# Performance work log

Hardware: AMD Instinct MI355X
Metric: run time of the kernel (lower is better)

The kernel has to match this reference:

```python
import jax, jax.numpy as jnp
import numpy as np

HIDDEN = 2048
N_HEADS = 16
N_KV_HEADS = 4
HEAD_DIM = 128
GROUPS = N_HEADS // N_KV_HEADS
MAX_SEQ = 2048
EPS = 1e-6
ROTARY_DIM = int(HEAD_DIM * 0.5)  # partial_rotary_factor = 0.5
ROPE_THETA = 10000.0


def _rms_norm(x, w):
    xf = x.astype(jnp.float32)
    normed = xf * jax.lax.rsqrt(jnp.mean(xf * xf, axis=-1, keepdims=True) + EPS)
    return (normed * (1.0 + w.astype(jnp.float32))).astype(x.dtype)


def _apply_rotary(x, cos, sin):
    half = x.shape[-1] // 2
    x1, x2 = x[..., :half], x[..., half:]
    return jnp.concatenate([x1 * cos - x2 * sin, x2 * cos + x1 * sin], axis=-1)


def setup_inputs() -> dict:
    key = jax.random.key(0)
    ks = jax.random.split(key, 6)
    s = 0.02
    return {
        "x": jax.random.normal(ks[0], (1, MAX_SEQ, HIDDEN), jnp.float32),
        "input_pos": jnp.arange(MAX_SEQ, dtype=jnp.int32),
        "wq": jax.random.normal(ks[1], (HIDDEN, N_HEADS * HEAD_DIM * 2), jnp.float32) * s,
        "wk": jax.random.normal(ks[2], (HIDDEN, N_KV_HEADS * HEAD_DIM), jnp.float32) * s,
        "wv": jax.random.normal(ks[3], (HIDDEN, N_KV_HEADS * HEAD_DIM), jnp.float32) * s,
        "wo": jax.random.normal(ks[4], (N_HEADS * HEAD_DIM, HIDDEN), jnp.float32) * s,
        "q_norm_w": jnp.zeros((HEAD_DIM,), jnp.float32),
        "k_norm_w": jnp.zeros((HEAD_DIM,), jnp.float32),
    }


def reference(x, input_pos, wq, wk, wv, wo, q_norm_w, k_norm_w):
    B, T, _ = x.shape
    dtype = x.dtype

    qg = (x @ wq).reshape(B, T, N_HEADS, HEAD_DIM * 2)
    q, gate = qg[..., :HEAD_DIM], qg[..., HEAD_DIM:]
    k = (x @ wk).reshape(B, T, N_KV_HEADS, HEAD_DIM)
    v = (x @ wv).reshape(B, T, N_KV_HEADS, HEAD_DIM)

    q = _rms_norm(q, q_norm_w)
    k = _rms_norm(k, k_norm_w)

    # partial RoPE on the first ROTARY_DIM channels of each head
    inv_freq = 1.0 / ROPE_THETA ** (
        jnp.arange(0, ROTARY_DIM, 2, dtype=jnp.float32) / ROTARY_DIM)
    freqs = jnp.outer(input_pos.astype(jnp.float32), inv_freq)  # [T, rd/2]
    cos = jnp.cos(freqs)[:, None, :]  # [T,1,rd/2] broadcast over heads
    sin = jnp.sin(freqs)[:, None, :]
    q = jnp.concatenate(
        [_apply_rotary(q[..., :ROTARY_DIM], cos, sin), q[..., ROTARY_DIM:]], axis=-1)
    k = jnp.concatenate(
        [_apply_rotary(k[..., :ROTARY_DIM], cos, sin), k[..., ROTARY_DIM:]], axis=-1)

    q = q.astype(dtype).transpose(0, 2, 1, 3)  # [B,H,T,D]
    k = k.astype(dtype).transpose(0, 2, 1, 3)  # [B,Hkv,T,D]
    v = v.transpose(0, 2, 1, 3)

    # KV-cache scatter update (cache starts at zeros)
    kc = jnp.zeros((1, N_KV_HEADS, MAX_SEQ, HEAD_DIM), dtype).at[:, :, input_pos].set(k)
    vc = jnp.zeros((1, N_KV_HEADS, MAX_SEQ, HEAD_DIM), dtype).at[:, :, input_pos].set(v)

    # GQA: group query heads instead of materializing repeated K/V
    qg_ = q.reshape(B, N_KV_HEADS, GROUPS, T, HEAD_DIM)
    scale = 1.0 / jnp.sqrt(jnp.asarray(HEAD_DIM, dtype))
    scores = jnp.einsum("bhgtd,bhsd->bhgts", qg_, kc) * scale  # [B,Hkv,G,T,S]

    mask = jnp.tril(jnp.ones((MAX_SEQ, MAX_SEQ), bool))[input_pos]  # [T,S]
    scores = jnp.where(mask[None, None, None], scores, jnp.finfo(scores.dtype).min)
    probs = jax.nn.softmax(scores, axis=-1)

    y = jnp.einsum("bhgts,bhsd->bhgtd", probs, vc)  # [B,Hkv,G,T,D]
    y = y.reshape(B, N_HEADS, T, HEAD_DIM).transpose(0, 2, 1, 3).reshape(B, T, -1)

    y = y * jax.nn.sigmoid(gate.reshape(B, T, -1))
    return y @ wo
```

## Files before the change

kernel.cpp:

```cpp
#include <hip/hip_runtime.h>
#include <cstdint>
#include <cmath>

using u16 = unsigned short;
typedef __attribute__((ext_vector_type(4))) short s16x4;
typedef __attribute__((ext_vector_type(8))) short s16x8;
typedef __attribute__((ext_vector_type(8))) __bf16 bf16x8;
typedef __attribute__((ext_vector_type(4))) float f32x4;

static __device__ __forceinline__ float b2f(u16 u) {
    unsigned int x = ((unsigned int)u) << 16;
    float f; __builtin_memcpy(&f, &x, 4); return f;
}
static __device__ __forceinline__ u16 f2b(float f) {
    unsigned int x; __builtin_memcpy(&x, &f, 4);
    x += 0x7FFFu + ((x >> 16) & 1u);
    return (u16)(x >> 16);
}
static __device__ __forceinline__ bf16x8 as_bf(s16x8 s) {
    return __builtin_bit_cast(bf16x8, s);
}

static __device__ __forceinline__ void stage16(const u16* g, u16* lds_base, int lane) {
#if __has_builtin(__builtin_amdgcn_global_load_lds)
    __builtin_amdgcn_global_load_lds((const __attribute__((address_space(1))) void*)g,
                                     (__attribute__((address_space(3))) void*)lds_base,
                                     16, 0, 0);
#else
    *(s16x8*)(lds_base + (size_t)lane * 8) = *(const s16x8*)g;
#endif
}

__global__ __launch_bounds__(256) void k_wtransAll(const float* __restrict__ wq,
                                                   const float* __restrict__ wk,
                                                   const float* __restrict__ wv,
                                                   const float* __restrict__ wo,
                                                   const float* __restrict__ x,
                                                   u16* __restrict__ wqkvT,
                                                   u16* __restrict__ woT,
                                                   u16* __restrict__ xb) {
    __shared__ u16 tile[64][72];
    int tx = blockIdx.x;
    int tid = threadIdx.x;
    if (tx >= 112) {
        int bid = (tx - 112) * 32 + blockIdx.y;
        int i = bid * 256 + tid;
        const int n4 = 2048 * 2048 / 4;
        const int stride = 1024 * 256;
        for (; i < n4; i += stride) {
            f32x4 v = ((const f32x4*)x)[i];
            s16x4 b;
            for (int j = 0; j < 4; ++j) b[j] = (short)f2b(v[j]);
            ((s16x4*)xb)[i] = b;
        }
        return;
    }
    const float* src; int N, nb, base; u16* dst;
    if (tx < 64)      { src = wq; N = 4096; nb = tx * 64;        base = tx * 64;               dst = wqkvT; }
    else if (tx < 72) { src = wk; N = 512;  nb = (tx - 64) * 64; base = 4096 + (tx - 64) * 64; dst = wqkvT; }
    else if (tx < 80) { src = wv; N = 512;  nb = (tx - 72) * 64; base = 4608 + (tx - 72) * 64; dst = wqkvT; }
    else              { src = wo; N = 2048; nb = (tx - 80) * 64; base = (tx - 80) * 64;        dst = woT; }
    int kb = blockIdx.y * 64;
    int kr = tid >> 2, c0 = (tid & 3) * 16;
#pragma unroll
    for (int i = 0; i < 4; ++i) {
        f32x4 v = *(const f32x4*)(src + (size_t)(kb + kr) * N + nb + c0 + i * 4);
        s16x4 b;
        for (int j = 0; j < 4; ++j) b[j] = (short)f2b(v[j]);
        *(s16x4*)&tile[kr][c0 + i * 4] = b;
    }
    __syncthreads();
    int nr = tid >> 2, k0 = (tid & 3) * 16;
    s16x8 v0, v1;
    for (int j = 0; j < 8; ++j) { v0[j] = (short)tile[k0 + j][nr]; v1[j] = (short)tile[k0 + 8 + j][nr]; }
    *(s16x8*)(dst + (size_t)(base + nr) * 2048 + kb + k0) = v0;
    *(s16x8*)(dst + (size_t)(base + nr) * 2048 + kb + k0 + 8) = v1;
}

template <bool OUT_F32>
__global__ __launch_bounds__(256) void k_gemm_bt(const u16* __restrict__ A,
                                                 const u16* __restrict__ Bt,
                                                 void* __restrict__ Cv,
                                                 int M, int N, int K) {
    __shared__ u16 As[128 * 64];
    __shared__ u16 Bs[128 * 64];
    int nx = gridDim.x, ny = gridDim.y;
    int flat = blockIdx.y * nx + blockIdx.x;
    int xcd = flat & 7, i = flat >> 3;
    int P = nx >> 3;
    int bnl = i / ny;
    int bmi = i - bnl * ny;
    if (bnl & 1) bmi = ny - 1 - bmi;
    int bn = (xcd * P + bnl) * 128;
    int bm = bmi * 128;

    int tid = threadIdx.x, wid = tid >> 6, lane = tid & 63;
    int l15 = lane & 15, g = lane >> 4;
    int wr = (wid >> 1) * 64, wc = (wid & 1) * 64;
    f32x4 acc[4][4];
    for (int ii = 0; ii < 4; ++ii) for (int j = 0; j < 4; ++j) acc[ii][j] = f32x4{0.f, 0.f, 0.f, 0.f};

    int srow = lane >> 3;
    int scol = ((lane & 7) * 8) ^ (srow << 3);
    const u16* pa = A + (size_t)(bm + srow) * K + scol;
    const u16* pb = Bt + (size_t)(bn + srow) * K + scol;

    for (int kb = 0; kb < K; kb += 64) {
        __syncthreads();
#pragma unroll
        for (int it = 0; it < 4; ++it) {
            int c = it * 4 + wid;
            stage16(pa + (size_t)(c * 8) * K + kb, &As[c * 512], lane);
            stage16(pb + (size_t)(c * 8) * K + kb, &Bs[c * 512], lane);
        }
        __syncthreads();
        int swz = (l15 & 7) << 4;
#pragma unroll
        for (int kk = 0; kk < 64; kk += 32) {
            bf16x8 af[4], bfr[4];
            for (int mi = 0; mi < 4; ++mi) {
                const char* rp = (const char*)As + (wr + mi * 16 + l15) * 128;
                af[mi] = as_bf(*(const s16x8*)(rp + ((kk * 2 + g * 16) ^ swz)));
            }
            for (int ni = 0; ni < 4; ++ni) {
                const char* rp = (const char*)Bs + (wc + ni * 16 + l15) * 128;
                bfr[ni] = as_bf(*(const s16x8*)(rp + ((kk * 2 + g * 16) ^ swz)));
            }
            for (int mi = 0; mi < 4; ++mi)
                for (int ni = 0; ni < 4; ++ni)
                    acc[mi][ni] = __builtin_amdgcn_mfma_f32_16x16x32_bf16(af[mi], bfr[ni], acc[mi][ni], 0, 0, 0);
        }
    }
    for (int mi = 0; mi < 4; ++mi)
        for (int ni = 0; ni < 4; ++ni) {
            int row = bm + wr + mi * 16 + g * 4;
            int col = bn + wc + ni * 16 + l15;
            for (int rr = 0; rr < 4; ++rr) {
                if (OUT_F32)
                    ((float*)Cv)[(size_t)(row + rr) * N + col] = acc[mi][ni][rr];
                else
                    ((u16*)Cv)[(size_t)(row + rr) * N + col] = f2b(acc[mi][ni][rr]);
            }
        }
}

__global__ __launch_bounds__(256) void k_prep_attn(u16* __restrict__ qkv,
                                                   const float* __restrict__ qw,
                                                   const float* __restrict__ kw,
                                                   const int* __restrict__ pos,
                                                   u16* __restrict__ vT) {
    __shared__ u16 tile[64][136];
    int bid = blockIdx.x;
    int tid = threadIdx.x;
    if (bid < 2048) {
        int t = bid, w = tid >> 6, l = tid & 63;
        float fp = (float)pos[t];
        int j = l & 31;
        float invf = __expf(-(float)j * (9.210340371976184f / 32.f));
        float sv, cv;
        sincosf(fp * invf, &sv, &cv);
        for (int task = w; task < 20; task += 4) {
            u16* p; const float* ww;
            if (task < 16) { p = qkv + (size_t)t * 5120 + task * 256; ww = qw; }
            else           { p = qkv + (size_t)t * 5120 + 4096 + (task - 16) * 128; ww = kw; }
            float v0 = b2f(p[l]), v1 = b2f(p[l + 64]);
            float ss = v0 * v0 + v1 * v1;
            for (int m = 32; m; m >>= 1) ss += __shfl_xor(ss, m);
            float rn = rsqrtf(ss * (1.f / 128.f) + 1e-6f);
            float q0 = v0 * rn * (1.f + ww[l]);
            float q1 = v1 * rn * (1.f + ww[l + 64]);
            float other = __shfl_xor(q0, 32);
            float ro = (l < 32) ? (q0 * cv - other * sv) : (q0 * cv + other * sv);
            p[l] = f2b(ro);
            p[l + 64] = f2b(q1);
        }
    } else {
        int r = bid - 2048;
        int tb = (r & 31) * 64, kvh = r >> 5;
        int tr = tid >> 2, c0 = (tid & 3) * 32;
        const u16* src = qkv + (size_t)(tb + tr) * 5120 + 4608 + kvh * 128 + c0;
#pragma unroll
        for (int i = 0; i < 4; ++i)
            *(s16x8*)&tile[tr][c0 + i * 8] = *(const s16x8*)(src + i * 8);
        __syncthreads();
        int d = tid >> 1, t0 = (tid & 1) * 32;
        u16* dst = vT + ((size_t)kvh * 128 + d) * 2048 + tb + t0;
#pragma unroll
        for (int i = 0; i < 4; ++i) {
            s16x8 v;
            for (int j = 0; j < 8; ++j) v[j] = (short)tile[t0 + i * 8 + j][d];
            *(s16x8*)(dst + i * 8) = v;
        }
    }
}

__global__ __launch_bounds__(256) void k_attn_split(const u16* __restrict__ qkv,
                                                    const u16* __restrict__ vT,
                                                    u16* __restrict__ po,
                                                    float* __restrict__ pl) {
    __shared__ u16 Kl[32 * 128];
    __shared__ u16 Vt[128][72];
    __shared__ u16 Pl[4][16][40];
    int head = blockIdx.y, kvh = head >> 2;
    int p = blockIdx.x >> 2, hf = blockIdx.x & 3;
    int tid = threadIdx.x, wid = tid >> 6, lane = tid & 63;
    int l15 = lane & 15, g = lane >> 4;

    for (int sub = 0; sub < 2; ++sub) {
        int qt = sub ? (31 - p) : p;
        int qb0 = qt * 64;
        int nk = (qt + 1) * 2;
        int ktb = (hf * nk) >> 2;
        int kte = ((hf + 1) * nk) >> 2;

        bf16x8 qf[4];
        {
            const u16* qp = qkv + (size_t)(qb0 + wid * 16 + l15) * 5120 + head * 256 + g * 8;
            for (int c = 0; c < 4; ++c) qf[c] = as_bf(*(const s16x8*)(qp + c * 32));
        }
        f32x4 oacc[8];
        for (int nb = 0; nb < 8; ++nb) oacc[nb] = f32x4{0.f, 0.f, 0.f, 0.f};
        float lsum[4] = {0.f, 0.f, 0.f, 0.f};

        for (int kt = ktb; kt < kte; ++kt) {
            int k0 = kt * 32;
            __syncthreads();
            {
#pragma unroll
                for (int i = 0; i < 2; ++i) {
                    int c = (wid << 1) | i;
                    int srow = (c << 2) + (lane >> 4);
                    int bofs = (((lane & 15) << 4) ^ ((srow & 7) << 4));
                    const u16* gs = (const u16*)((const char*)(qkv + (size_t)(k0 + srow) * 5120
                                                               + 4096 + kvh * 128) + bofs);
                    stage16(gs, &Kl[c * 512], lane);
                }
                int vr = tid >> 1, vc0 = (tid & 1) * 16;
                const u16* vs = vT + ((size_t)kvh * 128 + vr) * 2048 + k0 + vc0;
#pragma unroll
                for (int c = 0; c < 2; ++c)
                    *(s16x8*)&Vt[vr][vc0 + 8 * c] = *(const s16x8*)(vs + 8 * c);
            }
            __syncthreads();

            f32x4 sc2[2];
            sc2[0] = f32x4{0.f, 0.f, 0.f, 0.f}; sc2[1] = f32x4{0.f, 0.f, 0.f, 0.f};
            for (int h2 = 0; h2 < 2; ++h2) {
                int krow = h2 * 16 + l15;
                const char* kb_ = (const char*)Kl + krow * 256;
                int sw = (krow & 7) << 4;
                for (int c = 0; c < 4; ++c) {
                    bf16x8 kf = as_bf(*(const s16x8*)(kb_ + ((c * 64 + g * 16) ^ sw)));
                    sc2[h2] = __builtin_amdgcn_mfma_f32_16x16x32_bf16(qf[c], kf, sc2[h2], 0, 0, 0);
                }
            }
            const float scale = 0.08838834764831845f;
            for (int r = 0; r < 4; ++r) {
                int tq = qb0 + wid * 16 + g * 4 + r;
                float pv0 = (k0 + l15 > tq) ? 0.f : __expf(sc2[0][r] * scale);
                float pv1 = (k0 + 16 + l15 > tq) ? 0.f : __expf(sc2[1][r] * scale);
                Pl[wid][g * 4 + r][l15] = f2b(pv0);
                Pl[wid][g * 4 + r][16 + l15] = f2b(pv1);
                lsum[r] += pv0 + pv1;
            }
            bf16x8 pa = as_bf(*(const s16x8*)&Pl[wid][l15][g * 8]);
            for (int nb = 0; nb < 8; ++nb) {
                bf16x8 vb = as_bf(*(const s16x8*)&Vt[nb * 16 + l15][g * 8]);
                oacc[nb] = __builtin_amdgcn_mfma_f32_16x16x32_bf16(pa, vb, oacc[nb], 0, 0, 0);
            }
        }
        u16* pob = po + (size_t)hf * (2048 * 2048);
        float* plb = pl + hf * (16 * 2048) + head * 2048;
        for (int r = 0; r < 4; ++r) {
            float s = lsum[r];
            s += __shfl_xor(s, 1, 16); s += __shfl_xor(s, 2, 16);
            s += __shfl_xor(s, 4, 16); s += __shfl_xor(s, 8, 16);
            int row = qb0 + wid * 16 + g * 4 + r;
            if (l15 == 0) plb[row] = s;
            for (int nb = 0; nb < 8; ++nb)
                pob[(size_t)row * 2048 + head * 128 + nb * 16 + l15] = f2b(oacc[nb][r]);
        }
    }
}

__global__ __launch_bounds__(256) void k_combine(u16* __restrict__ po,
                                                 const float* __restrict__ pl,
                                                 const u16* __restrict__ qkv) {
    int t = blockIdx.x;
    int tid = threadIdx.x;
    int h = tid >> 4, d0 = (tid & 15) * 8;
    const size_t S = (size_t)2048 * 2048;
    const size_t base = (size_t)t * 2048 + h * 128 + d0;
    s16x8 a = *(const s16x8*)(po + base);
    s16x8 b = *(const s16x8*)(po + S + base);
    s16x8 c = *(const s16x8*)(po + 2 * S + base);
    s16x8 d = *(const s16x8*)(po + 3 * S + base);
    int li = h * 2048 + t;
    float l = pl[li] + pl[16 * 2048 + li] + pl[32 * 2048 + li] + pl[48 * 2048 + li];
    float inv = 1.f / l;
    s16x8 o;
    for (int j = 0; j < 8; ++j) {
        float y = (b2f((u16)a[j]) + b2f((u16)b[j]) + b2f((u16)c[j]) + b2f((u16)d[j])) * inv;
        float gt = b2f(qkv[(size_t)t * 5120 + h * 256 + 128 + d0 + j]);
        o[j] = (short)f2b(y / (1.f + __expf(-gt)));
    }
    *(s16x8*)(po + base) = o;
}

extern "C" void kernel_launch(void* const* d_in, const int* in_sizes, int n_in,
                              void* d_out, int out_size, void* d_ws, size_t ws_size,
                              hipStream_t stream) {
    const float* x   = (const float*)d_in[0];
    const int*   pos = (const int*)d_in[1];
    const float* wq  = (const float*)d_in[2];
    const float* wk  = (const float*)d_in[3];
    const float* wv  = (const float*)d_in[4];
    const float* wo  = (const float*)d_in[5];
    const float* qnw = (const float*)d_in[6];
    const float* knw = (const float*)d_in[7];
    float* out = (float*)d_out;
    char* ws = (char*)d_ws;

    u16*   qkv   = (u16*)(ws + 0);
    u16*   woT   = (u16*)(ws + 20971520);
    u16*   wqkvT = (u16*)(ws + 29360128);
    u16*   xb    = (u16*)(ws + 50331648);
    u16*   vTb   = (u16*)(ws + 29360128);
    u16*   pob   = (u16*)(ws + 31457280);
    float* plb   = (float*)(ws + 65011712);

    k_wtransAll<<<dim3(144, 32), 256, 0, stream>>>(wq, wk, wv, wo, x, wqkvT, woT, xb);

    k_gemm_bt<false><<<dim3(40, 16), 256, 0, stream>>>(xb, wqkvT, qkv, 2048, 5120, 2048);

    k_prep_attn<<<2176, 256, 0, stream>>>(qkv, qnw, knw, pos, vTb);

    k_attn_split<<<dim3(64, 16), 256, 0, stream>>>(qkv, vTb, pob, plb);
    k_combine<<<2048, 256, 0, stream>>>(pob, plb, qkv);

    k_gemm_bt<true><<<dim3(16, 16), 256, 0, stream>>>(pob, woT, out, 2048, 2048, 2048);
}
```

Measured before the change: 174.9 us.

## Fuse split-KV combine into attention kernel via last-block atomic counter

Removes the separate combine kernel. Each attention block bumps an atomic counter per (query-tile pair, head), and the fourth (last) block to finish sums the four partial outputs, normalises them by the summed row sums, applies the sigmoid gate and writes the result in place. The counters are zeroed inside the prep kernel. This saves one kernel launch and lets the combine overlap with attention blocks still running, at the cost of a threadfence and atomic per block plus a serial tail in the last block.

```diff
diff --git a/kernel.cpp b/kernel.cpp
--- a/kernel.cpp
+++ b/kernel.cpp
@@ -148,7 +148,8 @@
                                                    const float* __restrict__ qw,
                                                    const float* __restrict__ kw,
                                                    const int* __restrict__ pos,
-                                                   u16* __restrict__ vT) {
+                                                   u16* __restrict__ vT,
+                                                   unsigned int* __restrict__ cnt) {
     __shared__ u16 tile[64][136];
     int bid = blockIdx.x;
     int tid = threadIdx.x;
@@ -176,6 +177,7 @@
         }
     } else {
         int r = bid - 2048;
+        if (r == 0 && tid < 256) cnt[tid] = 0;
         int tb = (r & 31) * 64, kvh = r >> 5;
         int tr = tid >> 2, c0 = (tid & 3) * 32;
         const u16* src = qkv + (size_t)(tb + tr) * 5120 + 4608 + kvh * 128 + c0;
@@ -197,10 +199,12 @@
 __global__ __launch_bounds__(256) void k_attn_split(const u16* __restrict__ qkv,
                                                     const u16* __restrict__ vT,
                                                     u16* __restrict__ po,
-                                                    float* __restrict__ pl) {
+                                                    float* __restrict__ pl,
+                                                    unsigned int* __restrict__ cnt) {
     __shared__ u16 Kl[32 * 128];
     __shared__ u16 Vt[128][72];
     __shared__ u16 Pl[4][16][40];
+    __shared__ unsigned int old_s;
     int head = blockIdx.y, kvh = head >> 2;
     int p = blockIdx.x >> 2, hf = blockIdx.x & 3;
     int tid = threadIdx.x, wid = tid >> 6, lane = tid & 63;
@@ -281,30 +285,38 @@
                 pob[(size_t)row * 2048 + head * 128 + nb * 16 + l15] = f2b(oacc[nb][r]);
         }
     }
-}
-
-__global__ __launch_bounds__(256) void k_combine(u16* __restrict__ po,
-                                                 const float* __restrict__ pl,
-                                                 const u16* __restrict__ qkv) {
-    int t = blockIdx.x;
-    int tid = threadIdx.x;
-    int h = tid >> 4, d0 = (tid & 15) * 8;
-    const size_t S = (size_t)2048 * 2048;
-    const size_t base = (size_t)t * 2048 + h * 128 + d0;
-    s16x8 a = *(const s16x8*)(po + base);
-    s16x8 b = *(const s16x8*)(po + S + base);
-    s16x8 c = *(const s16x8*)(po + 2 * S + base);
-    s16x8 d = *(const s16x8*)(po + 3 * S + base);
-    int li = h * 2048 + t;
-    float l = pl[li] + pl[16 * 2048 + li] + pl[32 * 2048 + li] + pl[48 * 2048 + li];
-    float inv = 1.f / l;
-    s16x8 o;
-    for (int j = 0; j < 8; ++j) {
-        float y = (b2f((u16)a[j]) + b2f((u16)b[j]) + b2f((u16)c[j]) + b2f((u16)d[j])) * inv;
-        float gt = b2f(qkv[(size_t)t * 5120 + h * 256 + 128 + d0 + j]);
-        o[j] = (short)f2b(y / (1.f + __expf(-gt)));
-    }
-    *(s16x8*)(po + base) = o;
+
+    __threadfence();
+    __syncthreads();
+    if (tid == 0) old_s = atomicAdd(&cnt[p * 16 + head], 1u);
+    __syncthreads();
+    if (old_s == 3u) {
+        __threadfence();
+        const size_t S = (size_t)2048 * 2048;
+        for (int half = 0; half < 2; ++half) {
+            int qt = half ? (31 - p) : p;
+            int row = qt * 64 + (tid >> 2);
+            int c0 = (tid & 3) * 32;
+            size_t base = (size_t)row * 2048 + head * 128 + c0;
+            int li = head * 2048 + row;
+            float linv = 1.f / (pl[li] + pl[16 * 2048 + li] + pl[32 * 2048 + li] + pl[48 * 2048 + li]);
+#pragma unroll
+            for (int cc = 0; cc < 4; ++cc) {
+                s16x8 a = *(const s16x8*)(po + base + cc * 8);
+                s16x8 b = *(const s16x8*)(po + S + base + cc * 8);
+                s16x8 c = *(const s16x8*)(po + 2 * S + base + cc * 8);
+                s16x8 d = *(const s16x8*)(po + 3 * S + base + cc * 8);
+                s16x8 g8 = *(const s16x8*)(qkv + (size_t)row * 5120 + head * 256 + 128 + c0 + cc * 8);
+                s16x8 o;
+                for (int j = 0; j < 8; ++j) {
+                    float y = (b2f((u16)a[j]) + b2f((u16)b[j]) + b2f((u16)c[j]) + b2f((u16)d[j])) * linv;
+                    float gt = b2f((u16)g8[j]);
+                    o[j] = (short)f2b(y / (1.f + __expf(-gt)));
+                }
+                *(s16x8*)(po + base + cc * 8) = o;
+            }
+        }
+    }
 }
 
 extern "C" void kernel_launch(void* const* d_in, const int* in_sizes, int n_in,
@@ -328,15 +340,15 @@
     u16*   vTb   = (u16*)(ws + 29360128);
     u16*   pob   = (u16*)(ws + 31457280);
     float* plb   = (float*)(ws + 65011712);
+    unsigned int* cntb = (unsigned int*)(ws + 65536000);
 
     k_wtransAll<<<dim3(144, 32), 256, 0, stream>>>(wq, wk, wv, wo, x, wqkvT, woT, xb);
 
     k_gemm_bt<false><<<dim3(40, 16), 256, 0, stream>>>(xb, wqkvT, qkv, 2048, 5120, 2048);
 
-    k_prep_attn<<<2176, 256, 0, stream>>>(qkv, qnw, knw, pos, vTb);
-
-    k_attn_split<<<dim3(64, 16), 256, 0, stream>>>(qkv, vTb, pob, plb);
-    k_combine<<<2048, 256, 0, stream>>>(pob, plb, qkv);
+    k_prep_attn<<<2176, 256, 0, stream>>>(qkv, qnw, knw, pos, vTb, cntb);
+
+    k_attn_split<<<dim3(64, 16), 256, 0, stream>>>(qkv, vTb, pob, plb, cntb);
 
     k_gemm_bt<true><<<dim3(16, 16), 256, 0, stream>>>(pob, woT, out, 2048, 2048, 2048);
 }
```

New measurement: 427.0 us. 144% more time.
